# Performance work log

Hardware: AMD Instinct MI355X
Metric: run time of the kernel (lower is better)

The kernel has to match this reference:

```python
import jax, jax.numpy as jnp
import numpy as np

H = 64  # GRU hidden size


def _gru_scan(x_proj, m, U, b_rec):
    # x_proj: [S,B,3H] precomputed input projections (time-major); m: [S,B] bool mask
    B = x_proj.shape[1]
    h0 = jnp.zeros((B, H), x_proj.dtype)

    def step(h, inp):
        xp, mt = inp
        rec = h @ U + b_rec                       # [B,3H] (Keras reset_after=True)
        xz, xr, xh = jnp.split(xp, 3, axis=-1)
        rz, rr, rh = jnp.split(rec, 3, axis=-1)
        z = jax.nn.sigmoid(xz + rz)
        r = jax.nn.sigmoid(xr + rr)
        hh = jnp.tanh(xh + r * rh)
        hn = z * h + (1.0 - z) * hh
        hn = jnp.where(mt[:, None], hn, h)        # masked steps carry state through
        return hn, hn

    hT, hs = jax.lax.scan(step, h0, (x_proj, m))
    return hs, hT  # hs: [S,B,H], hT: [B,H]


def setup_inputs() -> dict:
    key = jax.random.key(0)
    ks = jax.random.split(key, 16)
    V, E = 50000, 25
    B, S, T = 512, 200, 10
    s = 0.05
    f32 = jnp.float32
    inp = {
        "input_batch": jax.random.randint(ks[0], (B, S, T), 0, V),
        "emb_table": jax.random.normal(ks[1], (V, E), f32) * s,
        "W_f": jax.random.normal(ks[2], (E, 3 * H), f32) * s,
        "U_f": jax.random.normal(ks[3], (H, 3 * H), f32) * s,
        "b_f": jnp.zeros((2, 3 * H), f32),
        "W_b": jax.random.normal(ks[4], (E, 3 * H), f32) * s,
        "U_b": jax.random.normal(ks[5], (H, 3 * H), f32) * s,
        "b_b": jnp.zeros((2, 3 * H), f32),
        "W_k": jax.random.normal(ks[6], (2 * H, H), f32) * s,
        "b_k": jnp.zeros((H,), f32),
        "W_q": jax.random.normal(ks[7], (H, H), f32) * s,
        "b_q": jnp.zeros((H,), f32),
        "W_e": jax.random.normal(ks[8], (H, 1), f32) * s,
        "b_e": jnp.zeros((1,), f32),
    }
    return inp


def reference(input_batch, emb_table, W_f, U_f, b_f, W_b, U_b, b_b, W_k, b_k, W_q, b_q, W_e, b_e):
    mask = input_batch != 0                                  # [B,S,T]
    emb = emb_table[input_batch]                             # [B,S,T,E]
    nm = mask.astype(emb.dtype)
    denom = nm.sum(axis=2)                                   # [B,S]
    denom = jnp.where(denom == 0, jnp.ones_like(denom), denom)
    x = (emb * nm[..., None]).sum(axis=2) / denom[..., None] # [B,S,E] masked mean over tags
    step_mask = mask[:, :, 0]                                # [B,S] GRU step mask

    xT = jnp.swapaxes(x, 0, 1)                               # [S,B,E]
    mT = jnp.swapaxes(step_mask, 0, 1)                       # [S,B]

    # forward GRU
    hs_f, hT_f = _gru_scan(xT @ W_f + b_f[0], mT, U_f, b_f[1])
    # backward GRU: reverse time, scan, reverse back
    hs_b, _ = _gru_scan((xT @ W_b + b_b[0])[::-1], mT[::-1], U_b, b_b[1])
    hs_b = hs_b[::-1]

    out = jnp.swapaxes(jnp.concatenate([hs_f, hs_b], axis=-1), 0, 1)  # [B,S,2H]

    # Bahdanau attention; query = forward final state
    keys = out @ W_k + b_k                                   # [B,S,H]
    queries = hT_f @ W_q + b_q                               # [B,H]
    e = jnp.tanh(keys + queries[:, None, :]) @ W_e + b_e     # [B,S,1]
    e = e + (1.0 - step_mask.astype(e.dtype))[..., None] * -1e9
    w = jax.nn.softmax(e, axis=1)                            # [B,S,1]
    context = (w * out).sum(axis=1)                          # [B,2H]
    return context
```

## Files before the change

### kernel.cpp

```cpp
#include <hip/hip_runtime.h>
#include <math.h>

#define BATCH 512
#define SEQ   200
#define TOK   10
#define EMB   25
#define HID   64
#define G3    192

__device__ __forceinline__ float fast_sigmoid(float t) {
    float e = __expf(-t);
    return __builtin_amdgcn_rcpf(1.f + e);
}
__device__ __forceinline__ float fast_tanh(float t) {
    float e2 = __expf(2.f * t);
    return 1.f - 2.f * __builtin_amdgcn_rcpf(e2 + 1.f);
}

#define LDS_BARRIER() do {                                   \
    asm volatile("s_waitcnt lgkmcnt(0)" ::: "memory");       \
    __builtin_amdgcn_s_barrier();                            \
    asm volatile("" ::: "memory");                           \
} while (0)

__global__ __launch_bounds__(256) void emb_mean_kernel(
    const int* __restrict__ ids_g, const float* __restrict__ emb,
    float* __restrict__ x, float* __restrict__ mask)
{
    int grp  = blockIdx.x * 8 + (threadIdx.x >> 5);
    int lane = threadIdx.x & 31;
    if (grp >= BATCH * SEQ) return;
    const int* ids = ids_g + (size_t)grp * TOK;
    float acc = 0.f;
    int cnt = 0;
    #pragma unroll
    for (int t = 0; t < TOK; t++) {
        int id = ids[t];
        if (id != 0) {
            cnt++;
            if (lane < EMB) acc += emb[(size_t)id * EMB + lane];
        }
    }
    if (lane < EMB)
        x[(size_t)grp * EMB + lane] = cnt ? acc / (float)cnt : 0.f;
    if (lane == 0)
        mask[grp] = (ids[0] != 0) ? 1.f : 0.f;
}

__global__ __launch_bounds__(192, 3) void gru_kernel(
    const float* __restrict__ xg, const float* __restrict__ maskg,
    const float* __restrict__ W_f, const float* __restrict__ U_f, const float* __restrict__ b_f,
    const float* __restrict__ W_b, const float* __restrict__ U_b, const float* __restrict__ b_b,
    float* __restrict__ outg, float* __restrict__ hT)
{
    const int bidx = blockIdx.x;
    const int dir  = bidx >> 9;
    const int b    = bidx & 511;
    const int tid  = threadIdx.x;
    const int w    = tid >> 6;
    const int j    = tid & 63;

    const float* W    = dir ? W_b : W_f;
    const float* U    = dir ? U_b : U_f;
    const float* bias = dir ? b_b : b_f;

    const int col = w * HID + j;

    float Ug[HID];
    #pragma unroll
    for (int k = 0; k < HID; k++) Ug[k] = U[k * G3 + col];
    float Wg[EMB];
    #pragma unroll
    for (int e = 0; e < EMB; e++) Wg[e] = W[e * G3 + col];
    const float bx = bias[col];
    const float br = bias[G3 + col];

    __shared__ float xs[SEQ * EMB];
    __shared__ float ms[SEQ];
    __shared__ float hs[HID];
    __shared__ float zs[HID];
    __shared__ float rs[HID];

    {
        const float4* xrow4 = (const float4*)(xg + (size_t)b * (SEQ * EMB));
        float4* xs4 = (float4*)xs;
        for (int i = tid; i < (SEQ * EMB) / 4; i += 192) xs4[i] = xrow4[i];
        for (int i = tid; i < SEQ; i += 192) ms[i] = maskg[(size_t)b * SEQ + i];
        if (tid < HID) hs[tid] = 0.f;
    }
    __syncthreads();

    float h = 0.f;
    float* obase = outg + (size_t)b * SEQ * (2 * HID) + dir * HID + j;

    float p;
    {
        const int s0 = dir ? (SEQ - 1) : 0;
        const float* xr = xs + s0 * EMB;
        float q0 = bx, q1 = 0.f;
        #pragma unroll
        for (int e = 0; e + 1 < EMB; e += 2) {
            q0 = fmaf(xr[e],     Wg[e],     q0);
            q1 = fmaf(xr[e + 1], Wg[e + 1], q1);
        }
        q0 = fmaf(xr[EMB - 1], Wg[EMB - 1], q0);
        p = q0 + q1;
    }

    for (int step = 0; step < SEQ; step++) {
        const int s = dir ? (SEQ - 1 - step) : step;

        float a0 = br, a1 = 0.f, a2 = 0.f, a3 = 0.f;
        #pragma unroll
        for (int k = 0; k < HID; k += 4) {
            a0 = fmaf(hs[k],     Ug[k],     a0);
            a1 = fmaf(hs[k + 1], Ug[k + 1], a1);
            a2 = fmaf(hs[k + 2], Ug[k + 2], a2);
            a3 = fmaf(hs[k + 3], Ug[k + 3], a3);
        }
        const float a = (a0 + a1) + (a2 + a3);

        if (w == 0)      zs[j] = fast_sigmoid(p + a);
        else if (w == 1) rs[j] = fast_sigmoid(p + a);

        LDS_BARRIER();

        if (w == 2) {
            float r  = rs[j];
            float z  = zs[j];
            float hh = fast_tanh(p + r * a);
            float hn = z * h + (1.f - z) * hh;
            hn = (ms[s] != 0.f) ? hn : h;
            h = hn;
            hs[j] = hn;
            obase[(size_t)s * (2 * HID)] = hn;
        }

        {
            const int sn  = dir ? (SEQ - 2 - step) : (step + 1);
            const int snc = (step + 1 < SEQ) ? sn : s;
            const float* xr = xs + snc * EMB;
            float q0 = bx, q1 = 0.f;
            #pragma unroll
            for (int e = 0; e + 1 < EMB; e += 2) {
                q0 = fmaf(xr[e],     Wg[e],     q0);
                q1 = fmaf(xr[e + 1], Wg[e + 1], q1);
            }
            q0 = fmaf(xr[EMB - 1], Wg[EMB - 1], q0);
            p = q0 + q1;
        }

        LDS_BARRIER();
    }
    if (w == 2 && dir == 0) hT[(size_t)b * HID + j] = h;
}

__global__ __launch_bounds__(256) void attn_kernel(
    const float* __restrict__ outg, const float* __restrict__ maskg,
    const float* __restrict__ hT,
    const float* __restrict__ W_k, const float* __restrict__ b_k,
    const float* __restrict__ W_q, const float* __restrict__ b_q,
    const float* __restrict__ W_e, const float* __restrict__ b_e,
    float* __restrict__ ctx)
{
    const int b   = blockIdx.x;
    const int tid = threadIdx.x;

    __shared__ float Wks[2 * HID * HID];
    __shared__ float qs[HID];
    __shared__ float es[SEQ];

    for (int i = tid; i < 2 * HID * HID; i += 256) Wks[i] = W_k[i];
    if (tid < HID) {
        float q = b_q[tid];
        const float* hrow = hT + (size_t)b * HID;
        #pragma unroll 8
        for (int i = 0; i < HID; i++) q = fmaf(hrow[i], W_q[i * HID + tid], q);
        qs[tid] = q;
    }
    __syncthreads();

    const int wave = tid >> 6;
    const int lane = tid & 63;
    const float bk = b_k[lane];
    const float we = W_e[lane];
    const float be = b_e[0];

    for (int s = wave; s < SEQ; s += 4) {
        const float* orow = outg + ((size_t)b * SEQ + s) * (2 * HID);
        float a0 = 0.f, a1 = 0.f, a2 = 0.f, a3 = 0.f;
        #pragma unroll
        for (int i = 0; i < 2 * HID; i += 4) {
            a0 = fmaf(orow[i + 0], Wks[(i + 0) * HID + lane], a0);
            a1 = fmaf(orow[i + 1], Wks[(i + 1) * HID + lane], a1);
            a2 = fmaf(orow[i + 2], Wks[(i + 2) * HID + lane], a2);
            a3 = fmaf(orow[i + 3], Wks[(i + 3) * HID + lane], a3);
        }
        float t = tanhf(((a0 + a1) + (a2 + a3)) + bk + qs[lane]) * we;
        #pragma unroll
        for (int off = 32; off > 0; off >>= 1) t += __shfl_down(t, off);
        if (lane == 0) {
            float pen = (maskg[(size_t)b * SEQ + s] != 0.f) ? 0.f : -1e9f;
            es[s] = t + be + pen;
        }
    }
    __syncthreads();

    if (tid < 64) {
        float mx = -1e30f;
        for (int s2 = tid; s2 < SEQ; s2 += 64) mx = fmaxf(mx, es[s2]);
        #pragma unroll
        for (int off = 32; off > 0; off >>= 1) mx = fmaxf(mx, __shfl_xor(mx, off));
        float sum = 0.f;
        for (int s2 = tid; s2 < SEQ; s2 += 64) {
            float w = expf(es[s2] - mx);
            es[s2] = w;
            sum += w;
        }
        #pragma unroll
        for (int off = 32; off > 0; off >>= 1) sum += __shfl_xor(sum, off);
        float inv = 1.f / sum;
        for (int s2 = tid; s2 < SEQ; s2 += 64) es[s2] *= inv;
    }
    __syncthreads();

    if (tid < 2 * HID) {
        const int jj = tid;
        float a0 = 0.f, a1 = 0.f;
        for (int s2 = 0; s2 < SEQ; s2 += 2) {
            a0 = fmaf(es[s2],     outg[((size_t)b * SEQ + s2)     * (2 * HID) + jj], a0);
            a1 = fmaf(es[s2 + 1], outg[((size_t)b * SEQ + s2 + 1) * (2 * HID) + jj], a1);
        }
        ctx[(size_t)b * (2 * HID) + jj] = a0 + a1;
    }
}

extern "C" void kernel_launch(void* const* d_in, const int* in_sizes, int n_in,
                              void* d_out, int out_size, void* d_ws, size_t ws_size,
                              hipStream_t stream) {
    const int*   ids = (const int*)  d_in[0];
    const float* emb = (const float*)d_in[1];
    const float* W_f = (const float*)d_in[2];
    const float* U_f = (const float*)d_in[3];
    const float* b_f = (const float*)d_in[4];
    const float* W_b = (const float*)d_in[5];
    const float* U_b = (const float*)d_in[6];
    const float* b_b = (const float*)d_in[7];
    const float* W_k = (const float*)d_in[8];
    const float* b_k = (const float*)d_in[9];
    const float* W_q = (const float*)d_in[10];
    const float* b_q = (const float*)d_in[11];
    const float* W_e = (const float*)d_in[12];
    const float* b_e = (const float*)d_in[13];

    float* ws   = (float*)d_ws;
    float* x    = ws;
    float* mask = ws + 2560000;
    float* out  = ws + 2662400;
    float* hT   = ws + 15769600;

    emb_mean_kernel<<<(BATCH * SEQ) / 8, 256, 0, stream>>>(ids, emb, x, mask);
    gru_kernel<<<1024, 192, 0, stream>>>(x, mask, W_f, U_f, b_f,
                                         W_b, U_b, b_b, out, hT);
    attn_kernel<<<BATCH, 256, 0, stream>>>(out, mask, hT, W_k, b_k,
                                           W_q, b_q, W_e, b_e, (float*)d_out);
}
```

Before: 435.5 us.

## Split GRU recurrence over K across six waves with LDS reduction

Each GRU block now uses 384 threads (six waves). Every wave owns a slice of the hidden dimension (K-split) and a slice of the embedding dimension, and computes partial sums for all three gates. The partials go to an LDS channel and wave 0 reduces them and applies the nonlinearities. This shortens the per-step serial FMA chain from 64 to 12, at the cost of extra LDS traffic, a serial reduction on one wave, and lower occupancy (launch_bounds 384,1). The x rows are padded to 28 floats so they can be read with float4 loads.

```diff
diff --git a/kernel.cpp b/kernel.cpp
--- a/kernel.cpp
+++ b/kernel.cpp
@@ -5,8 +5,10 @@
 #define SEQ   200
 #define TOK   10
 #define EMB   25
+#define XPAD  28
 #define HID   64
 #define G3    192
+#define NWAVE 6
 
 __device__ __forceinline__ float fast_sigmoid(float t) {
     float e = __expf(-t);
@@ -47,7 +49,30 @@
         mask[grp] = (ids[0] != 0) ? 1.f : 0.f;
 }
 
-__global__ __launch_bounds__(192, 3) void gru_kernel(
+
+#define UT_LIST(M) M(0) M(1) M(2) M(3) M(4) M(5) M(6) M(7) M(8) M(9) M(10) M(11)
+#define WT_LIST(M) M(0) M(1) M(2) M(3) M(4)
+
+#define DECL_UT(t) \
+    float uz##t = 0.f, ur##t = 0.f, uh##t = 0.f; \
+    if ((t) < nk) { const float* up_ = U + (size_t)(kstart + (t)) * G3 + j; \
+                    uz##t = up_[0]; ur##t = up_[HID]; uh##t = up_[2 * HID]; }
+
+#define DECL_WT(t) \
+    float wz##t = 0.f, wr##t = 0.f, wh##t = 0.f; \
+    if ((t) < ne) { const float* wp_ = W + (size_t)(estart + (t)) * G3 + j; \
+                    wz##t = wp_[0]; wr##t = wp_[HID]; wh##t = wp_[2 * HID]; }
+
+#define PIN3(a, b, c) asm volatile("" : "+v"(a), "+v"(b), "+v"(c))
+#define PIN_UT(t) PIN3(uz##t, ur##t, uh##t);
+#define PIN_WT(t) PIN3(wz##t, wr##t, wh##t);
+
+#define RECT(t, hk) { Z = fmaf(hk, uz##t, Z); R = fmaf(hk, ur##t, R); \
+                      HR = fmaf(hk, uh##t, HR); }
+#define XT(t, xe)   { nZ = fmaf(xe, wz##t, nZ); nR = fmaf(xe, wr##t, nR); \
+                      nHX = fmaf(xe, wh##t, nHX); }
+
+__global__ __launch_bounds__(384, 1) void gru_kernel(
     const float* __restrict__ xg, const float* __restrict__ maskg,
     const float* __restrict__ W_f, const float* __restrict__ U_f, const float* __restrict__ b_f,
     const float* __restrict__ W_b, const float* __restrict__ U_b, const float* __restrict__ b_b,
@@ -64,71 +89,82 @@
     const float* U    = dir ? U_b : U_f;
     const float* bias = dir ? b_b : b_f;
 
-    const int col = w * HID + j;
-
-    float Ug[HID];
-    #pragma unroll
-    for (int k = 0; k < HID; k++) Ug[k] = U[k * G3 + col];
-    float Wg[EMB];
-    #pragma unroll
-    for (int e = 0; e < EMB; e++) Wg[e] = W[e * G3 + col];
-    const float bx = bias[col];
-    const float br = bias[G3 + col];
-
-    __shared__ float xs[SEQ * EMB];
+    const int nk     = (w < 4) ? 12 : 8;
+    const int kstart = (w < 4) ? 12 * w : 48 + 8 * (w - 4);
+    const int ne     = (w < 5) ? 4 : 5;
+    const int estart = 4 * w;
+
+    __shared__ __align__(16) float xs[SEQ * XPAD];
     __shared__ float ms[SEQ];
-    __shared__ float hs[HID];
-    __shared__ float zs[HID];
-    __shared__ float rs[HID];
-
-    {
-        const float4* xrow4 = (const float4*)(xg + (size_t)b * (SEQ * EMB));
-        float4* xs4 = (float4*)xs;
-        for (int i = tid; i < (SEQ * EMB) / 4; i += 192) xs4[i] = xrow4[i];
-        for (int i = tid; i < SEQ; i += 192) ms[i] = maskg[(size_t)b * SEQ + i];
-        if (tid < HID) hs[tid] = 0.f;
-    }
+    __shared__ __align__(16) float hs[80];
+    __shared__ float chan[4][NWAVE][HID];
+
+    for (int i = tid; i < SEQ * EMB; i += 384) {
+        int s_ = i / EMB;
+        int e_ = i - s_ * EMB;
+        xs[s_ * XPAD + e_] = xg[(size_t)b * (SEQ * EMB) + i];
+    }
+    for (int i = tid; i < SEQ; i += 384) ms[i] = maskg[(size_t)b * SEQ + i];
+    if (tid < 80) hs[tid] = 0.f;
+
+    UT_LIST(DECL_UT)
+    WT_LIST(DECL_WT)
+    UT_LIST(PIN_UT)
+    WT_LIST(PIN_WT)
+
+    float bZ = 0.f, bR = 0.f, bHR = 0.f, bHX = 0.f;
+    if (w == 0) {
+        bZ  = bias[j] + bias[G3 + j];
+        bR  = bias[HID + j] + bias[G3 + HID + j];
+        bHX = bias[2 * HID + j];
+        bHR = bias[G3 + 2 * HID + j];
+    }
+
     __syncthreads();
 
+    const int sdelta = dir ? -1 : 1;
+    int s = dir ? (SEQ - 1) : 0;
     float h = 0.f;
     float* obase = outg + (size_t)b * SEQ * (2 * HID) + dir * HID + j;
 
-    float p;
+    float pxZ, pxR, pxHX;
     {
-        const int s0 = dir ? (SEQ - 1) : 0;
-        const float* xr = xs + s0 * EMB;
-        float q0 = bx, q1 = 0.f;
-        #pragma unroll
-        for (int e = 0; e + 1 < EMB; e += 2) {
-            q0 = fmaf(xr[e],     Wg[e],     q0);
-            q1 = fmaf(xr[e + 1], Wg[e + 1], q1);
-        }
-        q0 = fmaf(xr[EMB - 1], Wg[EMB - 1], q0);
-        p = q0 + q1;
+        const float* xrow = xs + s * XPAD;
+        float nZ = 0.f, nR = 0.f, nHX = 0.f;
+        const float4 xa = *(const float4*)(xrow + estart);
+        XT(0, xa.x) XT(1, xa.y) XT(2, xa.z) XT(3, xa.w)
+        if (ne == 5) { float x4 = xrow[estart + 4]; XT(4, x4) }
+        pxZ = nZ; pxR = nR; pxHX = nHX;
     }
 
     for (int step = 0; step < SEQ; step++) {
-        const int s = dir ? (SEQ - 1 - step) : step;
-
-        float a0 = br, a1 = 0.f, a2 = 0.f, a3 = 0.f;
-        #pragma unroll
-        for (int k = 0; k < HID; k += 4) {
-            a0 = fmaf(hs[k],     Ug[k],     a0);
-            a1 = fmaf(hs[k + 1], Ug[k + 1], a1);
-            a2 = fmaf(hs[k + 2], Ug[k + 2], a2);
-            a3 = fmaf(hs[k + 3], Ug[k + 3], a3);
-        }
-        const float a = (a0 + a1) + (a2 + a3);
-
-        if (w == 0)      zs[j] = fast_sigmoid(p + a);
-        else if (w == 1) rs[j] = fast_sigmoid(p + a);
+        float Z = pxZ, R = pxR, HX = pxHX, HR = 0.f;
+        {
+            const float4* hv = (const float4*)(hs + kstart);
+            const float4 ha = hv[0], hb = hv[1], hc = hv[2];
+            RECT(0, ha.x) RECT(1, ha.y) RECT(2,  ha.z) RECT(3,  ha.w)
+            RECT(4, hb.x) RECT(5, hb.y) RECT(6,  hb.z) RECT(7,  hb.w)
+            RECT(8, hc.x) RECT(9, hc.y) RECT(10, hc.z) RECT(11, hc.w)
+        }
+        chan[0][w][j] = Z;
+        chan[1][w][j] = R;
+        chan[2][w][j] = HR;
+        chan[3][w][j] = HX;
 
         LDS_BARRIER();
 
-        if (w == 2) {
-            float r  = rs[j];
-            float z  = zs[j];
-            float hh = fast_tanh(p + r * a);
+        if (w == 0) {
+            float sZ = bZ, sR = bR, sHR = bHR, sHX = bHX;
+            #pragma unroll
+            for (int t = 0; t < NWAVE; t++) {
+                sZ  += chan[0][t][j];
+                sR  += chan[1][t][j];
+                sHR += chan[2][t][j];
+                sHX += chan[3][t][j];
+            }
+            float z  = fast_sigmoid(sZ);
+            float r  = fast_sigmoid(sR);
+            float hh = fast_tanh(sHX + r * sHR);
             float hn = z * h + (1.f - z) * hh;
             hn = (ms[s] != 0.f) ? hn : h;
             h = hn;
@@ -137,22 +173,19 @@
         }
 
         {
-            const int sn  = dir ? (SEQ - 2 - step) : (step + 1);
-            const int snc = (step + 1 < SEQ) ? sn : s;
-            const float* xr = xs + snc * EMB;
-            float q0 = bx, q1 = 0.f;
-            #pragma unroll
-            for (int e = 0; e + 1 < EMB; e += 2) {
-                q0 = fmaf(xr[e],     Wg[e],     q0);
-                q1 = fmaf(xr[e + 1], Wg[e + 1], q1);
-            }
-            q0 = fmaf(xr[EMB - 1], Wg[EMB - 1], q0);
-            p = q0 + q1;
+            const int sn = (step < SEQ - 1) ? s + sdelta : s;
+            const float* xrow = xs + sn * XPAD;
+            float nZ = 0.f, nR = 0.f, nHX = 0.f;
+            const float4 xa = *(const float4*)(xrow + estart);
+            XT(0, xa.x) XT(1, xa.y) XT(2, xa.z) XT(3, xa.w)
+            if (ne == 5) { float x4 = xrow[estart + 4]; XT(4, x4) }
+            pxZ = nZ; pxR = nR; pxHX = nHX;
+            s = sn;
         }
 
         LDS_BARRIER();
     }
-    if (w == 2 && dir == 0) hT[(size_t)b * HID + j] = h;
+    if (w == 0 && dir == 0) hT[(size_t)b * HID + j] = h;
 }
 
 __global__ __launch_bounds__(256) void attn_kernel(
@@ -260,7 +293,7 @@
     float* hT   = ws + 15769600;
 
     emb_mean_kernel<<<(BATCH * SEQ) / 8, 256, 0, stream>>>(ids, emb, x, mask);
-    gru_kernel<<<1024, 192, 0, stream>>>(x, mask, W_f, U_f, b_f,
+    gru_kernel<<<1024, 384, 0, stream>>>(x, mask, W_f, U_f, b_f,
                                          W_b, U_b, b_b, out, hT);
     attn_kernel<<<BATCH, 256, 0, stream>>>(out, mask, hT, W_k, b_k,
                                            W_q, b_q, W_e, b_e, (float*)d_out);
```

Result: slower. 505.2 us (+16.0%).
